# Optimization experiments

Measured on AMD Instinct MI355X. Metric: run time of the kernel, lower is better.

The kernel has to match this reference:

```python
import jax, jax.numpy as jnp
import numpy as np

T, D_IN, D_OUT, E = 4096, 1024, 4096, 8


def setup_inputs() -> dict:
    key = jax.random.key(0)
    k1, k2, k3 = jax.random.split(key, 3)
    input_tensor = jax.random.normal(k1, (T, D_IN), dtype=jnp.float32)
    # tokens are pre-sorted by expert; contiguous counts per expert (sum == T)
    expert_token_cnt = jnp.full((E,), T // E, dtype=jnp.int32)
    # learned params: nn.init.normal_(mean=0, std=1)
    weight = jax.random.normal(k2, (E, D_OUT, D_IN), dtype=jnp.float32)
    bias = jax.random.normal(k3, (E, D_OUT), dtype=jnp.float32)
    return {"input_tensor": input_tensor, "expert_token_cnt": expert_token_cnt,
            "weight": weight, "bias": bias}


def reference(input_tensor, expert_token_cnt, weight, bias):
    # Grouped GEMM: token t in segment e computes y[t] = x[t] @ W[e].T + b[e]
    # followed by exact (erf) GELU. dropout_rate = 0.0 -> identity.
    n_tok = input_tensor.shape[0]
    n_exp = weight.shape[0]
    bounds = jnp.cumsum(expert_token_cnt)                       # [E]
    expert_id = jnp.searchsorted(bounds, jnp.arange(n_tok), side='right')  # [T]
    onehot = (expert_id[:, None] == jnp.arange(n_exp)[None, :]).astype(input_tensor.dtype)  # [T,E]
    y = jnp.zeros((n_tok, weight.shape[1]), dtype=input_tensor.dtype)
    for e in range(n_exp):  # fixed small expert count; each iter is one masked GEMM
        xe = input_tensor * onehot[:, e][:, None]               # zero out other experts' tokens
        y = y + jnp.einsum('ti,oi->to', xe, weight[e])
    y = y + bias[expert_id]                                     # per-token expert bias
    y = jax.nn.gelu(y, approximate=False)                       # torch default exact GELU
    return y
```

## Files before the change

### kernel.cpp

```cpp
#include <hip/hip_runtime.h>
#include <hip/hip_bf16.h>
#include <math.h>

#define T_TOK 4096
#define DIN   1024
#define DOUT  4096
#define NEXP  8

#define BM 128
#define BN 128
#define BK 32

typedef __bf16 bf16x8 __attribute__((ext_vector_type(8)));
typedef float  f32x4  __attribute__((ext_vector_type(4)));

__device__ __forceinline__ unsigned short f2bf(float f) {
    union { float f; unsigned u; } x; x.f = f;
    unsigned r = x.u + 0x7FFFu + ((x.u >> 16) & 1u);
    return (unsigned short)(r >> 16);
}

__global__ __launch_bounds__(256) void convert_f32_bf16(
        const float* __restrict__ src, unsigned short* __restrict__ dst, int n4) {
    int i = blockIdx.x * blockDim.x + threadIdx.x;
    int stride = gridDim.x * blockDim.x;
    const float4* s4 = (const float4*)src;
    ushort4* d4 = (ushort4*)dst;
    for (; i < n4; i += stride) {
        float4 v = s4[i];
        ushort4 o;
        o.x = f2bf(v.x); o.y = f2bf(v.y); o.z = f2bf(v.z); o.w = f2bf(v.w);
        d4[i] = o;
    }
}

__device__ __forceinline__ void gload_lds16(const __bf16* g, __bf16* l) {
    __builtin_amdgcn_global_load_lds(
        (const __attribute__((address_space(1))) unsigned int*)g,
        (__attribute__((address_space(3))) unsigned int*)l,
        16, 0, 0);
}

__global__ __launch_bounds__(256) void moe_gemm(
        const __bf16* __restrict__ A, const __bf16* __restrict__ W,
        const float* __restrict__ bias, const int* __restrict__ cnt,
        float* __restrict__ C) {
    __shared__ __bf16 Asm[BM * BK];
    __shared__ __bf16 Bsm[BN * BK];

    const int tid  = threadIdx.x;
    const int wid  = tid >> 6;
    const int lane = tid & 63;

    const int n_tiles = DOUT / BN;
    const int mt = blockIdx.x / n_tiles;
    const int nt = blockIdx.x % n_tiles;
    const int m0 = mt * BM;
    const int n0 = nt * BN;

    int e = 0, csum = 0;
    #pragma unroll
    for (int i = 0; i < NEXP; ++i) {
        int c = cnt[i];
        if (m0 >= csum + c) { csum += c; e = i + 1; }
    }

    const __bf16* Ab = A + (size_t)m0 * DIN;
    const __bf16* Wb = W + (size_t)e * DOUT * DIN + (size_t)n0 * DIN;

    const int srow  = wid * 16 + (lane >> 2);
    const int skcol = (lane & 3) * 8;

    const int wr = wid >> 1, wc = wid & 1;
    const int fr = lane & 15;
    const int fk = (lane >> 4) * 8;

    f32x4 acc[4][4];
    #pragma unroll
    for (int i = 0; i < 4; ++i)
        #pragma unroll
        for (int j = 0; j < 4; ++j)
            acc[i][j] = (f32x4)(0.0f);

    for (int kt = 0; kt < DIN; kt += BK) {
        #pragma unroll
        for (int s = 0; s < 2; ++s) {
            gload_lds16(Ab + (size_t)(s * 64 + srow) * DIN + kt + skcol,
                        &Asm[(s * 64 + wid * 16) * BK]);
            gload_lds16(Wb + (size_t)(s * 64 + srow) * DIN + kt + skcol,
                        &Bsm[(s * 64 + wid * 16) * BK]);
        }
        __syncthreads();

        bf16x8 af[4], bfr[4];
        #pragma unroll
        for (int i = 0; i < 4; ++i)
            af[i] = *(const bf16x8*)&Asm[(wr * 64 + i * 16 + fr) * BK + fk];
        #pragma unroll
        for (int j = 0; j < 4; ++j)
            bfr[j] = *(const bf16x8*)&Bsm[(wc * 64 + j * 16 + fr) * BK + fk];

        #pragma unroll
        for (int i = 0; i < 4; ++i)
            #pragma unroll
            for (int j = 0; j < 4; ++j)
                acc[i][j] = __builtin_amdgcn_mfma_f32_16x16x32_bf16(
                                af[i], bfr[j], acc[i][j], 0, 0, 0);
        __syncthreads();
    }

    const int colf = lane & 15;
    const int rowf = (lane >> 4) * 4;
    #pragma unroll
    for (int j = 0; j < 4; ++j) {
        const int col = n0 + wc * 64 + j * 16 + colf;
        const float bv = bias[(size_t)e * DOUT + col];
        #pragma unroll
        for (int i = 0; i < 4; ++i) {
            #pragma unroll
            for (int r = 0; r < 4; ++r) {
                const int row = m0 + wr * 64 + i * 16 + rowf + r;
                float x = acc[i][j][r] + bv;
                float g = 0.5f * x * (1.0f + erff(x * 0.70710678118654752f));
                C[(size_t)row * DOUT + col] = g;
            }
        }
    }
}

extern "C" void kernel_launch(void* const* d_in, const int* in_sizes, int n_in,
                              void* d_out, int out_size, void* d_ws, size_t ws_size,
                              hipStream_t stream) {
    (void)in_sizes; (void)n_in; (void)out_size; (void)ws_size;
    const float* input  = (const float*)d_in[0];
    const int*   cnt    = (const int*)d_in[1];
    const float* weight = (const float*)d_in[2];
    const float* bias   = (const float*)d_in[3];
    float* out = (float*)d_out;

    unsigned short* a_bf = (unsigned short*)d_ws;
    unsigned short* w_bf = a_bf + (size_t)T_TOK * DIN;

    const int n4_in = T_TOK * DIN / 4;
    const int n4_w  = NEXP * DOUT * DIN / 4;
    hipLaunchKernelGGL(convert_f32_bf16, dim3(1024), dim3(256), 0, stream,
                       input, a_bf, n4_in);
    hipLaunchKernelGGL(convert_f32_bf16, dim3(2048), dim3(256), 0, stream,
                       weight, w_bf, n4_w);

    dim3 grid((T_TOK / BM) * (DOUT / BN));
    hipLaunchKernelGGL(moe_gemm, grid, dim3(256), 0, stream,
                       (const __bf16*)a_bf, (const __bf16*)w_bf, bias, cnt, out);
}
```

Baseline: 298.3 us.

## Fuse weight bf16 conversion into GEMM with double-buffered swizzled LDS

Drops the separate pass that converts all expert weights to bf16. The GEMM now loads fp32 weights into registers, converts them, and writes them to LDS. It also raises BK to 64, double-buffers A and B in LDS with the next tile prefetched during compute, and XOR-swizzles the LDS layout to avoid bank conflicts. This removes a full write and read of the 128MB weight tensor, but each GEMM block now reads fp32 weights, so weight traffic per block doubles and register pressure rises.

```diff
diff --git a/kernel.cpp b/kernel.cpp
--- a/kernel.cpp
+++ b/kernel.cpp
@@ -9,10 +9,12 @@
 
 #define BM 128
 #define BN 128
-#define BK 32
+#define BK 64
+#define NT (DIN / BK)
 
 typedef __bf16 bf16x8 __attribute__((ext_vector_type(8)));
 typedef float  f32x4  __attribute__((ext_vector_type(4)));
+typedef unsigned short u16x8 __attribute__((ext_vector_type(8)));
 
 __device__ __forceinline__ unsigned short f2bf(float f) {
     union { float f; unsigned u; } x; x.f = f;
@@ -41,12 +43,12 @@
         16, 0, 0);
 }
 
-__global__ __launch_bounds__(256) void moe_gemm(
-        const __bf16* __restrict__ A, const __bf16* __restrict__ W,
+__global__ __launch_bounds__(256, 2) void moe_gemm_fused(
+        const __bf16* __restrict__ A, const float* __restrict__ W,
         const float* __restrict__ bias, const int* __restrict__ cnt,
         float* __restrict__ C) {
-    __shared__ __bf16 Asm[BM * BK];
-    __shared__ __bf16 Bsm[BN * BK];
+    __shared__ __bf16 Asm[2][BM * BK];
+    __shared__ __bf16 Bsm[2][BN * BK];
 
     const int tid  = threadIdx.x;
     const int wid  = tid >> 6;
@@ -66,14 +68,45 @@
     }
 
     const __bf16* Ab = A + (size_t)m0 * DIN;
-    const __bf16* Wb = W + (size_t)e * DOUT * DIN + (size_t)n0 * DIN;
+    const float*  Wb = W + (size_t)e * DOUT * DIN + (size_t)n0 * DIN;
 
-    const int srow  = wid * 16 + (lane >> 2);
-    const int skcol = (lane & 3) * 8;
+    const int srow = lane >> 3;
+    const int sg   = lane & 7;
+    const int sgx  = sg ^ srow;
 
-    const int wr = wid >> 1, wc = wid & 1;
-    const int fr = lane & 15;
-    const int fk = (lane >> 4) * 8;
+    auto stage_A = [&](int b, int kt) {
+        #pragma unroll
+        for (int s = 0; s < 4; ++s) {
+            int rowL = wid * 32 + s * 8 + srow;
+            gload_lds16(Ab + (size_t)rowL * DIN + kt + sgx * 8,
+                        &Asm[b][(wid * 32 + s * 8) * BK]);
+        }
+    };
+    auto load_W = [&](f32x4* wr, int kt) {
+        #pragma unroll
+        for (int s = 0; s < 4; ++s) {
+            int rowL = wid * 32 + s * 8 + srow;
+            const float* p = Wb + (size_t)rowL * DIN + kt + sg * 8;
+            wr[s * 2]     = *(const f32x4*)p;
+            wr[s * 2 + 1] = *(const f32x4*)(p + 4);
+        }
+    };
+    auto write_B = [&](int b, const f32x4* wr) {
+        #pragma unroll
+        for (int s = 0; s < 4; ++s) {
+            int rowL = wid * 32 + s * 8 + srow;
+            u16x8 v;
+            #pragma unroll
+            for (int q = 0; q < 4; ++q) v[q]     = f2bf(wr[s * 2][q]);
+            #pragma unroll
+            for (int q = 0; q < 4; ++q) v[4 + q] = f2bf(wr[s * 2 + 1][q]);
+            *(u16x8*)&Bsm[b][rowL * BK + sgx * 8] = v;
+        }
+    };
+
+    const int wr_ = wid >> 1, wc_ = wid & 1;
+    const int fr  = lane & 15;
+    const int fh  = lane >> 4;
 
     f32x4 acc[4][4];
     #pragma unroll
@@ -82,44 +115,60 @@
         for (int j = 0; j < 4; ++j)
             acc[i][j] = (f32x4)(0.0f);
 
-    for (int kt = 0; kt < DIN; kt += BK) {
+    auto compute = [&](int b) {
         #pragma unroll
-        for (int s = 0; s < 2; ++s) {
-            gload_lds16(Ab + (size_t)(s * 64 + srow) * DIN + kt + skcol,
-                        &Asm[(s * 64 + wid * 16) * BK]);
-            gload_lds16(Wb + (size_t)(s * 64 + srow) * DIN + kt + skcol,
-                        &Bsm[(s * 64 + wid * 16) * BK]);
+        for (int ks = 0; ks < 2; ++ks) {
+            bf16x8 af[4], bf[4];
+            #pragma unroll
+            for (int i = 0; i < 4; ++i) {
+                int r = wr_ * 64 + i * 16 + fr;
+                int g = (ks * 4 + fh) ^ (r & 7);
+                af[i] = *(const bf16x8*)&Asm[b][r * BK + g * 8];
+            }
+            #pragma unroll
+            for (int j = 0; j < 4; ++j) {
+                int r = wc_ * 64 + j * 16 + fr;
+                int g = (ks * 4 + fh) ^ (r & 7);
+                bf[j] = *(const bf16x8*)&Bsm[b][r * BK + g * 8];
+            }
+            #pragma unroll
+            for (int i = 0; i < 4; ++i)
+                #pragma unroll
+                for (int j = 0; j < 4; ++j)
+                    acc[i][j] = __builtin_amdgcn_mfma_f32_16x16x32_bf16(
+                                    af[i], bf[j], acc[i][j], 0, 0, 0);
         }
+    };
+
+    f32x4 wreg[8];
+    load_W(wreg, 0);
+    stage_A(0, 0);
+    write_B(0, wreg);
+    __syncthreads();
+
+    int cur = 0;
+    for (int t = 0; t < NT - 1; ++t) {
+        const int ktn = (t + 1) * BK;
+        load_W(wreg, ktn);
+        stage_A(cur ^ 1, ktn);
+        compute(cur);
+        write_B(cur ^ 1, wreg);
         __syncthreads();
-
-        bf16x8 af[4], bfr[4];
-        #pragma unroll
-        for (int i = 0; i < 4; ++i)
-            af[i] = *(const bf16x8*)&Asm[(wr * 64 + i * 16 + fr) * BK + fk];
-        #pragma unroll
-        for (int j = 0; j < 4; ++j)
-            bfr[j] = *(const bf16x8*)&Bsm[(wc * 64 + j * 16 + fr) * BK + fk];
-
-        #pragma unroll
-        for (int i = 0; i < 4; ++i)
-            #pragma unroll
-            for (int j = 0; j < 4; ++j)
-                acc[i][j] = __builtin_amdgcn_mfma_f32_16x16x32_bf16(
-                                af[i], bfr[j], acc[i][j], 0, 0, 0);
-        __syncthreads();
+        cur ^= 1;
     }
+    compute(cur);
 
     const int colf = lane & 15;
     const int rowf = (lane >> 4) * 4;
     #pragma unroll
     for (int j = 0; j < 4; ++j) {
-        const int col = n0 + wc * 64 + j * 16 + colf;
+        const int col = n0 + wc_ * 64 + j * 16 + colf;
         const float bv = bias[(size_t)e * DOUT + col];
         #pragma unroll
         for (int i = 0; i < 4; ++i) {
             #pragma unroll
             for (int r = 0; r < 4; ++r) {
-                const int row = m0 + wr * 64 + i * 16 + rowf + r;
+                const int row = m0 + wr_ * 64 + i * 16 + rowf + r;
                 float x = acc[i][j][r] + bv;
                 float g = 0.5f * x * (1.0f + erff(x * 0.70710678118654752f));
                 C[(size_t)row * DOUT + col] = g;
@@ -139,16 +188,12 @@
     float* out = (float*)d_out;
 
     unsigned short* a_bf = (unsigned short*)d_ws;
-    unsigned short* w_bf = a_bf + (size_t)T_TOK * DIN;
 
     const int n4_in = T_TOK * DIN / 4;
-    const int n4_w  = NEXP * DOUT * DIN / 4;
     hipLaunchKernelGGL(convert_f32_bf16, dim3(1024), dim3(256), 0, stream,
                        input, a_bf, n4_in);
-    hipLaunchKernelGGL(convert_f32_bf16, dim3(2048), dim3(256), 0, stream,
-                       weight, w_bf, n4_w);
 
     dim3 grid((T_TOK / BM) * (DOUT / BN));
-    hipLaunchKernelGGL(moe_gemm, grid, dim3(256), 0, stream,
-                       (const __bf16*)a_bf, (const __bf16*)w_bf, bias, cnt, out);
+    hipLaunchKernelGGL(moe_gemm_fused, grid, dim3(256), 0, stream,
+                       (const __bf16*)a_bf, weight, bias, cnt, out);
 }
```

Result: slower. 309.1 us (+3.6%).

## Double BK, XOR-swizzle LDS tiles, and fuse conversion kernels into one

Applied to the files above, without the earlier changes.

Raises the K tile from 32 to 64 so each barrier pair covers two MFMA k-steps. Loads into LDS use an XOR swizzle on 16-byte groups, and the fragment reads apply the same swizzle, to avoid bank conflicts. The two fp32-to-bf16 conversion launches become one kernel that writes 8 elements per thread. The cost is larger LDS tiles and more complex addressing.

```diff
diff --git a/kernel.cpp b/kernel.cpp
--- a/kernel.cpp
+++ b/kernel.cpp
@@ -9,10 +9,11 @@
 
 #define BM 128
 #define BN 128
-#define BK 32
+#define BK 64
 
 typedef __bf16 bf16x8 __attribute__((ext_vector_type(8)));
 typedef float  f32x4  __attribute__((ext_vector_type(4)));
+typedef unsigned short u16x8 __attribute__((ext_vector_type(8)));
 
 __device__ __forceinline__ unsigned short f2bf(float f) {
     union { float f; unsigned u; } x; x.f = f;
@@ -20,17 +21,23 @@
     return (unsigned short)(r >> 16);
 }
 
-__global__ __launch_bounds__(256) void convert_f32_bf16(
-        const float* __restrict__ src, unsigned short* __restrict__ dst, int n4) {
+__global__ __launch_bounds__(256) void convert_all(
+        const float* __restrict__ srcA, unsigned short* __restrict__ dstA,
+        const float* __restrict__ srcW, unsigned short* __restrict__ dstW) {
+    const int nA = T_TOK * DIN / 8;
+    const int nW = NEXP * DOUT * DIN / 8;
     int i = blockIdx.x * blockDim.x + threadIdx.x;
-    int stride = gridDim.x * blockDim.x;
-    const float4* s4 = (const float4*)src;
-    ushort4* d4 = (ushort4*)dst;
-    for (; i < n4; i += stride) {
-        float4 v = s4[i];
-        ushort4 o;
-        o.x = f2bf(v.x); o.y = f2bf(v.y); o.z = f2bf(v.z); o.w = f2bf(v.w);
-        d4[i] = o;
+    const int stride = gridDim.x * blockDim.x;
+    for (; i < nA + nW; i += stride) {
+        const float* s; unsigned short* d; int idx;
+        if (i < nA) { s = srcA; d = dstA; idx = i; }
+        else        { s = srcW; d = dstW; idx = i - nA; }
+        const f32x4* p = (const f32x4*)(s + (size_t)idx * 8);
+        f32x4 v0 = p[0], v1 = p[1];
+        u16x8 o;
+        #pragma unroll
+        for (int q = 0; q < 4; ++q) { o[q] = f2bf(v0[q]); o[4 + q] = f2bf(v1[q]); }
+        *(u16x8*)(d + (size_t)idx * 8) = o;
     }
 }
 
@@ -68,12 +75,12 @@
     const __bf16* Ab = A + (size_t)m0 * DIN;
     const __bf16* Wb = W + (size_t)e * DOUT * DIN + (size_t)n0 * DIN;
 
-    const int srow  = wid * 16 + (lane >> 2);
-    const int skcol = (lane & 3) * 8;
+    const int srow = lane >> 3;
+    const int sgx  = (lane & 7) ^ srow;
 
-    const int wr = wid >> 1, wc = wid & 1;
-    const int fr = lane & 15;
-    const int fk = (lane >> 4) * 8;
+    const int wr_ = wid >> 1, wc_ = wid & 1;
+    const int fr  = lane & 15;
+    const int fh  = lane >> 4;
 
     f32x4 acc[4][4];
     #pragma unroll
@@ -84,28 +91,37 @@
 
     for (int kt = 0; kt < DIN; kt += BK) {
         #pragma unroll
-        for (int s = 0; s < 2; ++s) {
-            gload_lds16(Ab + (size_t)(s * 64 + srow) * DIN + kt + skcol,
-                        &Asm[(s * 64 + wid * 16) * BK]);
-            gload_lds16(Wb + (size_t)(s * 64 + srow) * DIN + kt + skcol,
-                        &Bsm[(s * 64 + wid * 16) * BK]);
+        for (int s = 0; s < 4; ++s) {
+            const int rbase = wid * 32 + s * 8;
+            gload_lds16(Ab + (size_t)(rbase + srow) * DIN + kt + sgx * 8,
+                        &Asm[rbase * BK]);
+            gload_lds16(Wb + (size_t)(rbase + srow) * DIN + kt + sgx * 8,
+                        &Bsm[rbase * BK]);
         }
         __syncthreads();
 
-        bf16x8 af[4], bfr[4];
         #pragma unroll
-        for (int i = 0; i < 4; ++i)
-            af[i] = *(const bf16x8*)&Asm[(wr * 64 + i * 16 + fr) * BK + fk];
-        #pragma unroll
-        for (int j = 0; j < 4; ++j)
-            bfr[j] = *(const bf16x8*)&Bsm[(wc * 64 + j * 16 + fr) * BK + fk];
-
-        #pragma unroll
-        for (int i = 0; i < 4; ++i)
+        for (int ks = 0; ks < 2; ++ks) {
+            bf16x8 af[4], bf[4];
             #pragma unroll
-            for (int j = 0; j < 4; ++j)
-                acc[i][j] = __builtin_amdgcn_mfma_f32_16x16x32_bf16(
-                                af[i], bfr[j], acc[i][j], 0, 0, 0);
+            for (int i = 0; i < 4; ++i) {
+                const int r = wr_ * 64 + i * 16 + fr;
+                const int g = (ks * 4 + fh) ^ (r & 7);
+                af[i] = *(const bf16x8*)&Asm[r * BK + g * 8];
+            }
+            #pragma unroll
+            for (int j = 0; j < 4; ++j) {
+                const int r = wc_ * 64 + j * 16 + fr;
+                const int g = (ks * 4 + fh) ^ (r & 7);
+                bf[j] = *(const bf16x8*)&Bsm[r * BK + g * 8];
+            }
+            #pragma unroll
+            for (int i = 0; i < 4; ++i)
+                #pragma unroll
+                for (int j = 0; j < 4; ++j)
+                    acc[i][j] = __builtin_amdgcn_mfma_f32_16x16x32_bf16(
+                                    af[i], bf[j], acc[i][j], 0, 0, 0);
+        }
         __syncthreads();
     }
 
@@ -113,13 +129,13 @@
     const int rowf = (lane >> 4) * 4;
     #pragma unroll
     for (int j = 0; j < 4; ++j) {
-        const int col = n0 + wc * 64 + j * 16 + colf;
+        const int col = n0 + wc_ * 64 + j * 16 + colf;
         const float bv = bias[(size_t)e * DOUT + col];
         #pragma unroll
         for (int i = 0; i < 4; ++i) {
             #pragma unroll
             for (int r = 0; r < 4; ++r) {
-                const int row = m0 + wr * 64 + i * 16 + rowf + r;
+                const int row = m0 + wr_ * 64 + i * 16 + rowf + r;
                 float x = acc[i][j][r] + bv;
                 float g = 0.5f * x * (1.0f + erff(x * 0.70710678118654752f));
                 C[(size_t)row * DOUT + col] = g;
@@ -141,12 +157,8 @@
     unsigned short* a_bf = (unsigned short*)d_ws;
     unsigned short* w_bf = a_bf + (size_t)T_TOK * DIN;
 
-    const int n4_in = T_TOK * DIN / 4;
-    const int n4_w  = NEXP * DOUT * DIN / 4;
-    hipLaunchKernelGGL(convert_f32_bf16, dim3(1024), dim3(256), 0, stream,
-                       input, a_bf, n4_in);
-    hipLaunchKernelGGL(convert_f32_bf16, dim3(2048), dim3(256), 0, stream,
-                       weight, w_bf, n4_w);
+    hipLaunchKernelGGL(convert_all, dim3(2048), dim3(256), 0, stream,
+                       input, a_bf, weight, w_bf);
 
     dim3 grid((T_TOK / BM) * (DOUT / BN));
     hipLaunchKernelGGL(moe_gemm, grid, dim3(256), 0, stream,
```

After: 298.2 us. Within noise of the previous version (-0.0%).
